# Optimization experiments

Hardware: AMD Instinct MI355X
Metric: run time of the kernel (lower is better)

Reference implementation:

```python
import jax, jax.numpy as jnp
import numpy as np

B, C, HK, WK = 1, 128, 32, 32
S = 4                       # upsample factor hq/hk = dilation
HQ, WQ = HK * S, WK * S
NH = 4                      # heads
HD = C // NH                # head dim
KH = KW = 7                 # odd(max(3, round(2*0.1*32)))
DH = DW = S
EPS = float(jnp.finfo(jnp.float32).eps)  # torch RMSNorm default eps for fp32


def natten_indices(L, K, D):
    """NATTEN clamped-window key indices per query position. Returns [L, K] int array."""
    NS = K // 2
    i = np.arange(L)
    if D <= 1:
        start = np.maximum(i - NS, 0) + (i + NS >= L) * (L - i - NS - 1)
    else:
        ni = i - NS * D
        imodd = i % D
        a = (L // D) * D
        b = L - a
        far = np.where(imodd < b, L - b + imodd - 2 * NS * D, a + imodd - K * D)
        start = np.where(ni < 0, imodd, np.where(i + NS * D >= L, far, ni))
    return jnp.asarray(start[:, None] + np.arange(K)[None, :] * D)


def setup_inputs() -> dict:
    key = jax.random.key(0)
    ks = jax.random.split(key, 8)
    sc = 1.0 / np.sqrt(C)
    return {
        "q": jax.random.normal(ks[0], (B, C, HQ, WQ), jnp.float32),
        "k": jax.random.normal(ks[1], (B, C, HK, WK), jnp.float32),
        "v": jax.random.normal(ks[2], (B, C, HK, WK), jnp.float32),
        "conv_w": jax.random.normal(ks[3], (C, C, 3, 3), jnp.float32) * (sc / 3.0),
        "normq_w": 1.0 + 0.02 * jax.random.normal(ks[4], (C,), jnp.float32),
        "normk_w": 1.0 + 0.02 * jax.random.normal(ks[5], (C,), jnp.float32),
        "qproj_w": jax.random.normal(ks[6], (C, C), jnp.float32) * sc,
        "qproj_b": jnp.zeros((C,), jnp.float32),
        "kproj_w": jax.random.normal(ks[7], (C, C), jnp.float32) * sc,
        "kproj_b": jnp.zeros((C,), jnp.float32),
    }


def _rmsnorm(x, w):  # x: [B,C,H,W]; RMS over channel dim
    ms = jnp.mean(x * x, axis=1, keepdims=True)
    return x * jax.lax.rsqrt(ms + EPS) * w[None, :, None, None]


def reference(q, k, v, conv_w, normq_w, normk_w, qproj_w, qproj_b, kproj_w, kproj_b):
    # 3x3 conv on q (no bias, padding=1)
    q = jax.lax.conv_general_dilated(q, conv_w, (1, 1), "SAME",
                                     dimension_numbers=("NCHW", "OIHW", "NCHW"))
    q = _rmsnorm(q, normq_w)
    k = _rmsnorm(k, normk_w)
    # 1x1 projections (Conv2d k=1 with bias)
    q = jnp.einsum("oc,bchw->bohw", qproj_w, q) + qproj_b[None, :, None, None]
    k = jnp.einsum("oc,bchw->bohw", kproj_w, k) + kproj_b[None, :, None, None]
    # nearest-exact upsample of k, v to (HQ, WQ); integer factor -> exact pixel repeat
    k = jnp.repeat(jnp.repeat(k, S, axis=2), S, axis=3)
    v = jnp.repeat(jnp.repeat(v, S, axis=2), S, axis=3)
    # NATTEN layout [B, H, W, heads, hd]
    qn = q.reshape(B, NH, HD, HQ, WQ).transpose(0, 3, 4, 1, 2)
    kn = k.reshape(B, NH, HD, HQ, WQ).transpose(0, 3, 4, 1, 2)
    vh = v.transpose(0, 2, 3, 1)  # [B,HQ,WQ,C]; V is shared (expanded) across heads.
    # channel-pad-to-8 in the original is a no-op here since C % 8 == 0.
    ih = natten_indices(HQ, KH, DH)  # [HQ, KH]
    iw = natten_indices(WQ, KW, DW)  # [WQ, KW]
    k_nb = jnp.take(jnp.take(kn, ih, axis=1), iw, axis=3)  # [B,HQ,KH,WQ,KW,NH,HD]
    v_nb = jnp.take(jnp.take(vh, ih, axis=1), iw, axis=3)  # [B,HQ,KH,WQ,KW,C]
    scale = HD ** -0.5
    logits = jnp.einsum("bijhd,bimjnhd->bijhmn", qn, k_nb) * scale
    attn = jax.nn.softmax(logits.reshape(B, HQ, WQ, NH, KH * KW), axis=-1)
    attn = attn.reshape(B, HQ, WQ, NH, KH, KW)
    # heads share V, and the block takes mean over heads at the end; the mean
    # commutes with the (linear) V-contraction, so average attention first.
    attn_mean = attn.mean(axis=3)  # [B,HQ,WQ,KH,KW]
    out = jnp.einsum("bijmn,bimjnc->bcij", attn_mean, v_nb)  # [B,C,HQ,WQ]
    return out
```

## Files before the change

kernel.cpp:

```cpp
#include <hip/hip_runtime.h>

#define EPS_ 1.1920928955078125e-07f
#define SCALE_ 0.17677669529663687f

typedef __attribute__((ext_vector_type(8))) short s8b;
typedef __attribute__((ext_vector_type(4))) float f32x4;

static __device__ __forceinline__ unsigned short f2bf(float f) {
  unsigned int u = __float_as_uint(f);
  unsigned int r = (u + 0x7fffu + ((u >> 16) & 1u)) >> 16;
  return (unsigned short)r;
}
static __device__ __forceinline__ float b2fs(short h) {
  return __uint_as_float(((unsigned int)(unsigned short)h) << 16);
}
static __device__ __forceinline__ int S_(int c) {
  return (c < 3) ? 0 : ((c > 28) ? 25 : (c - 3));
}

__global__ __launch_bounds__(256) void prep_k(
    const float* __restrict__ q_in, const float* __restrict__ k_in,
    const float* __restrict__ conv_w, const float* __restrict__ normq_w,
    const float* __restrict__ normk_w, const float* __restrict__ qproj_w,
    const float* __restrict__ kproj_w, const float* __restrict__ kbias,
    unsigned short* __restrict__ qb, unsigned short* __restrict__ kpb,
    unsigned short* __restrict__ wb, unsigned short* __restrict__ wnq) {
  __shared__ __align__(16) char smem[53504];
  unsigned short* t_l = (unsigned short*)smem;
  unsigned short* x_l = (unsigned short*)smem;
  unsigned short* wnk_l = (unsigned short*)(smem + 17408);
  float* red_l = (float*)(smem + 52224);
  float* rs_l  = (float*)(smem + 53248);
  const int b = blockIdx.x, tid = threadIdx.x;
  const int w = tid >> 6, lane = tid & 63;
  const int lm = lane & 15, kg = lane >> 4;

  if (b < 256) {
    const int px0 = b * 64;
    for (int i = tid; i < 2048; i += 256) {
      int c = i >> 4, f = i & 15;
      float4 v = *(const float4*)&q_in[c * 16384 + px0 + f * 4];
      t_l[(f * 4 + 0) * 136 + c] = f2bf(v.x);
      t_l[(f * 4 + 1) * 136 + c] = f2bf(v.y);
      t_l[(f * 4 + 2) * 136 + c] = f2bf(v.z);
      t_l[(f * 4 + 3) * 136 + c] = f2bf(v.w);
    }
    __syncthreads();
    for (int i = tid; i < 1024; i += 256) {
      int p = i >> 4, s = i & 15;
      int px = px0 + p;
      int opx = px + 2 * (px >> 7) + 131;
      *(s8b*)&qb[opx * 128 + s * 8] = *(const s8b*)&t_l[p * 136 + s * 8];
    }
  } else if (b < 265) {
    int gid = (b - 256) * 256 + tid;
    s8b z = {0, 0, 0, 0, 0, 0, 0, 0};
    for (int j = gid; j < 2080; j += 2304) {
      *(s8b*)&qb[j * 8] = z;
      *(s8b*)&qb[129 * 130 * 128 + j * 8] = z;
    }
    for (int j = gid; j < 2048; j += 2304) {
      int r = (j >> 4) + 1, s = j & 15;
      *(s8b*)&qb[(r * 130) * 128 + s * 8] = z;
      *(s8b*)&qb[(r * 130 + 129) * 128 + s * 8] = z;
    }
  } else if (b < 281) {
    const int px0 = (b - 265) * 64;
    for (int i = tid; i < 2048; i += 256) {
      int c = i >> 4, f = i & 15;
      float4 v = *(const float4*)&k_in[c * 1024 + px0 + f * 4];
      x_l[(f * 4 + 0) * 136 + c] = f2bf(v.x);
      x_l[(f * 4 + 1) * 136 + c] = f2bf(v.y);
      x_l[(f * 4 + 2) * 136 + c] = f2bf(v.z);
      x_l[(f * 4 + 3) * 136 + c] = f2bf(v.w);
    }
    for (int i = tid; i < 16384; i += 256) {
      int o = i >> 7, c = i & 127;
      wnk_l[o * 136 + c] = f2bf(kproj_w[i] * normk_w[c]);
    }
    __syncthreads();
    {
      int px = tid >> 2, t4 = tid & 3;
      float ssum = 0.f;
#pragma unroll
      for (int j = 0; j < 4; j++) {
        s8b v = *(const s8b*)&x_l[px * 136 + t4 * 32 + j * 8];
#pragma unroll
        for (int e = 0; e < 8; e++) { float f = b2fs(v[e]); ssum += f * f; }
      }
      red_l[px * 4 + t4] = ssum;
    }
    __syncthreads();
    if (tid < 64)
      rs_l[tid] = rsqrtf((red_l[4 * tid] + red_l[4 * tid + 1] + red_l[4 * tid + 2] +
                          red_l[4 * tid + 3]) * (1.f / 128.f) + EPS_);
    __syncthreads();
    f32x4 acc[2][4];
#pragma unroll
    for (int a = 0; a < 2; a++)
#pragma unroll
      for (int n = 0; n < 4; n++) acc[a][n] = (f32x4){0.f, 0.f, 0.f, 0.f};
#pragma unroll
    for (int kc = 0; kc < 4; kc++) {
      s8b a0 = *(const s8b*)&wnk_l[(2 * w * 16 + lm) * 136 + kc * 32 + kg * 8];
      s8b a1 = *(const s8b*)&wnk_l[((2 * w + 1) * 16 + lm) * 136 + kc * 32 + kg * 8];
#pragma unroll
      for (int nt = 0; nt < 4; nt++) {
        s8b bf = *(const s8b*)&x_l[(nt * 16 + lm) * 136 + kc * 32 + kg * 8];
        acc[0][nt] = __builtin_amdgcn_mfma_f32_16x16x32_bf16(a0, bf, acc[0][nt], 0, 0, 0);
        acc[1][nt] = __builtin_amdgcn_mfma_f32_16x16x32_bf16(a1, bf, acc[1][nt], 0, 0, 0);
      }
    }
    __syncthreads();
#pragma unroll
    for (int mi = 0; mi < 2; mi++)
#pragma unroll
      for (int nt = 0; nt < 4; nt++)
#pragma unroll
        for (int r = 0; r < 4; r++) {
          int px = nt * 16 + lm, c = (2 * w + mi) * 16 + kg * 4 + r;
          x_l[px * 136 + c] = f2bf(kbias[c] + rs_l[px] * acc[mi][nt][r]);
        }
    __syncthreads();
    for (int i = tid; i < 1024; i += 256) {
      int px = i >> 4, s = i & 15;
      *(s8b*)&kpb[(px0 + px) * 128 + s * 8] = *(const s8b*)&x_l[px * 136 + s * 8];
    }
  } else {
    int idx = (b - 281) * 256 + tid;
    if (idx < 147456) {
      int i32 = idx & 31, r = idx >> 5;
      int oc = r & 127, r2 = r >> 7;
      int kc = r2 & 3, t = r2 >> 2;
      wb[idx] = f2bf(conv_w[oc * 1152 + (kc * 32 + i32) * 9 + t]);
    } else {
      int j = idx - 147456;
      wnq[j] = f2bf(qproj_w[j] * normq_w[j & 127]);
    }
  }
}

__global__ __launch_bounds__(512) void fused_k(
    const unsigned short* __restrict__ qb, const unsigned short* __restrict__ kpb,
    const float* __restrict__ v_in, const unsigned short* __restrict__ wb,
    const unsigned short* __restrict__ wnq, const float* __restrict__ qbias,
    float* __restrict__ out) {
  __shared__ __align__(16) char smem[65344];
  unsigned short* in_l = (unsigned short*)smem;
  unsigned short* qc_l = (unsigned short*)smem;
  unsigned short* a_l  = (unsigned short*)smem;
  float* o_l   = (float*)smem;
  unsigned short* kx_l = (unsigned short*)(smem + 27200);
  unsigned short* v_l  = (unsigned short*)(smem + 44608);
  float* red_l = (float*)(smem + 63040);
  float* rs_l  = (float*)(smem + 65088);

  const int tid = threadIdx.x;
  const int CY = blockIdx.x >> 4, CX = blockIdx.x & 15;
  const int Y0 = CY * 8, X0 = CX * 8;
  const int w = tid >> 6, lane = tid & 63;
  const int lm = lane & 15, kg = lane >> 4;
  const int mg = w & 1, ng = w >> 1;
  const int h = w >> 1, mh = w & 1;

  const int sy0 = S_(2 * CY), sy1 = S_(2 * CY + 1);
  const int sx0 = S_(2 * CX), sx1 = S_(2 * CX + 1);
  const int kyb = min(sy0, 24), kxb = min(sx0, 24);
  const int oy0 = sy0 - kyb, oy1 = sy1 - kyb;
  const int ox0 = sx0 - kxb, ox1 = sx1 - kxb;

  for (int i = tid; i < 1600; i += 512) {
    int s = i & 15, r = i >> 4;
    int ry = r / 10, rx = r - ry * 10;
    *(s8b*)&in_l[r * 136 + s * 8] =
        *(const s8b*)&qb[((Y0 + ry) * 130 + X0 + rx) * 128 + s * 8];
  }
  for (int i = tid; i < 1024; i += 512) {
    int j = i >> 4, s = i & 15;
    int ky = j >> 3, kx = j & 7;
    *(s8b*)&kx_l[j * 136 + s * 8] =
        *(const s8b*)&kpb[((kyb + ky) * 32 + kxb + kx) * 128 + s * 8];
  }
  {
    const int j = tid & 63, cg = tid >> 6;
    const int ky = j >> 3, kx = j & 7;
    const float* vp = &v_in[(kyb + ky) * 32 + kxb + kx];
#pragma unroll
    for (int it = 0; it < 16; it++) {
      int c = cg * 16 + it;
      v_l[c * 72 + j] = f2bf(vp[c * 1024]);
    }
  }
  __syncthreads();

  f32x4 acc[4];
#pragma unroll
  for (int a = 0; a < 4; a++) acc[a] = (f32x4){0.f, 0.f, 0.f, 0.f};
  const int pxc = ng * 16 + lm;
  const int qy = pxc >> 3, qx = pxc & 7;
#pragma unroll
  for (int t = 0; t < 9; t++) {
    const int dy = t / 3, dx = t - (t / 3) * 3;
#pragma unroll
    for (int kc = 0; kc < 4; kc++) {
      const unsigned short* wp = wb + (t * 4 + kc) * 4096;
      s8b af[4];
#pragma unroll
      for (int mt = 0; mt < 4; mt++)
        af[mt] = *(const s8b*)&wp[((mg * 4 + mt) * 16 + lm) * 32 + kg * 8];
      s8b bf = *(const s8b*)&in_l[((qy + dy) * 10 + qx + dx) * 136 + kc * 32 + kg * 8];
#pragma unroll
      for (int mt = 0; mt < 4; mt++)
        acc[mt] = __builtin_amdgcn_mfma_f32_16x16x32_bf16(af[mt], bf, acc[mt], 0, 0, 0);
    }
  }
  __syncthreads();
#pragma unroll
  for (int mt = 0; mt < 4; mt++)
#pragma unroll
    for (int r = 0; r < 4; r++) {
      int c = (mg * 4 + mt) * 16 + kg * 4 + r;
      qc_l[pxc * 136 + c] = f2bf(acc[mt][r]);
    }
  __syncthreads();

  {
    int px = tid >> 3, t8 = tid & 7;
    const unsigned short* row = &qc_l[px * 136 + t8 * 16];
    s8b v0 = *(const s8b*)row;
    s8b v1 = *(const s8b*)(row + 8);
    float s = 0.f;
#pragma unroll
    for (int e = 0; e < 8; e++) {
      float f0 = b2fs(v0[e]), f1 = b2fs(v1[e]);
      s += f0 * f0 + f1 * f1;
    }
    red_l[px * 8 + t8] = s;
  }
  __syncthreads();
  if (tid < 64) {
    float s = 0.f;
#pragma unroll
    for (int e = 0; e < 8; e++) s += red_l[tid * 8 + e];
    rs_l[tid] = rsqrtf(s * (1.f / 128.f) + EPS_);
  }
  __syncthreads();

  {
    f32x4 qa[4];
#pragma unroll
    for (int a = 0; a < 4; a++) qa[a] = (f32x4){0.f, 0.f, 0.f, 0.f};
#pragma unroll
    for (int kc = 0; kc < 4; kc++) {
      s8b af[4];
#pragma unroll
      for (int mt = 0; mt < 4; mt++)
        af[mt] = *(const s8b*)&wnq[((mg * 4 + mt) * 16 + lm) * 128 + kc * 32 + kg * 8];
      s8b bf = *(const s8b*)&qc_l[pxc * 136 + kc * 32 + kg * 8];
#pragma unroll
      for (int mt = 0; mt < 4; mt++)
        qa[mt] = __builtin_amdgcn_mfma_f32_16x16x32_bf16(af[mt], bf, qa[mt], 0, 0, 0);
    }
    __syncthreads();
    const float rs = rs_l[pxc];
#pragma unroll
    for (int mt = 0; mt < 4; mt++)
#pragma unroll
      for (int r = 0; r < 4; r++) {
        int c = (mg * 4 + mt) * 16 + kg * 4 + r;
        qc_l[pxc * 136 + c] = f2bf(qbias[c] + rs * qa[mt][r]);
      }
  }
  __syncthreads();

  f32x4 lg[2][4];
  {
    s8b qa[2], kb[4];
#pragma unroll
    for (int mt = 0; mt < 2; mt++)
      qa[mt] = *(const s8b*)&qc_l[((mh * 2 + mt) * 16 + lm) * 136 + h * 32 + kg * 8];
#pragma unroll
    for (int nt = 0; nt < 4; nt++)
      kb[nt] = *(const s8b*)&kx_l[(nt * 16 + lm) * 136 + h * 32 + kg * 8];
#pragma unroll
    for (int mt = 0; mt < 2; mt++)
#pragma unroll
      for (int nt = 0; nt < 4; nt++)
        lg[mt][nt] = __builtin_amdgcn_mfma_f32_16x16x32_bf16(
            qa[mt], kb[nt], (f32x4){0.f, 0.f, 0.f, 0.f}, 0, 0, 0);
  }
  __syncthreads();

  {
    const int kyA = lm >> 3, kxq = lm & 7;
    const bool kxv0 = (unsigned)(kxq - ox0) < 7u;
    const bool kxv1 = (unsigned)(kxq - ox1) < 7u;
#pragma unroll
    for (int mt = 0; mt < 2; mt++) {
#pragma unroll
      for (int r = 0; r < 4; r++) {
        int j = (mh * 2 + mt) * 16 + kg * 4 + r;
        int oy = ((j >> 5) & 1) ? oy1 : oy0;
        bool kxv = ((j >> 2) & 1) ? kxv1 : kxv0;
        float l[4];
#pragma unroll
        for (int nt = 0; nt < 4; nt++) {
          int ky = 2 * nt + kyA;
          bool valid = kxv && ((unsigned)(ky - oy) < 7u);
          l[nt] = valid ? lg[mt][nt][r] * SCALE_ : -1e30f;
        }
        float mx = fmaxf(fmaxf(l[0], l[1]), fmaxf(l[2], l[3]));
#pragma unroll
        for (int off = 1; off < 16; off <<= 1) mx = fmaxf(mx, __shfl_xor(mx, off, 64));
        float e0 = __expf(l[0] - mx), e1 = __expf(l[1] - mx);
        float e2 = __expf(l[2] - mx), e3 = __expf(l[3] - mx);
        float ss = e0 + e1 + e2 + e3;
#pragma unroll
        for (int off = 1; off < 16; off <<= 1) ss += __shfl_xor(ss, off, 64);
        float inv = 1.f / ss;
        unsigned short* ap = &a_l[(h * 64 + j) * 72];
        ap[lm]      = f2bf(e0 * inv);
        ap[16 + lm] = f2bf(e1 * inv);
        ap[32 + lm] = f2bf(e2 * inv);
        ap[48 + lm] = f2bf(e3 * inv);
      }
    }
  }
  __syncthreads();

  f32x4 oacc[4];
#pragma unroll
  for (int a = 0; a < 4; a++) oacc[a] = (f32x4){0.f, 0.f, 0.f, 0.f};
#pragma unroll
  for (int kc = 0; kc < 2; kc++) {
    s8b vb2 = *(const s8b*)&v_l[(w * 16 + lm) * 72 + kc * 32 + kg * 8];
#pragma unroll
    for (int hh = 0; hh < 4; hh++) {
#pragma unroll
      for (int mt = 0; mt < 4; mt++) {
        s8b pa = *(const s8b*)&a_l[(hh * 64 + mt * 16 + lm) * 72 + kc * 32 + kg * 8];
        oacc[mt] = __builtin_amdgcn_mfma_f32_16x16x32_bf16(pa, vb2, oacc[mt], 0, 0, 0);
      }
    }
  }
  __syncthreads();

#pragma unroll
  for (int mt = 0; mt < 4; mt++)
#pragma unroll
    for (int r = 0; r < 4; r++)
      o_l[(w * 16 + lm) * 68 + mt * 16 + kg * 4 + r] = 0.25f * oacc[mt][r];
  __syncthreads();
  for (int i = tid; i < 2048; i += 512) {
    int c = i >> 4, rr = i & 15;
    int qyo = rr >> 1, hx = rr & 1;
    float4 v = *(const float4*)&o_l[c * 68 + qyo * 8 + hx * 4];
    *(float4*)&out[c * 16384 + (Y0 + qyo) * 128 + X0 + hx * 4] = v;
  }
}

extern "C" void kernel_launch(void* const* d_in, const int* in_sizes, int n_in,
                              void* d_out, int out_size, void* d_ws, size_t ws_size,
                              hipStream_t stream) {
  const float* q_in    = (const float*)d_in[0];
  const float* k_in    = (const float*)d_in[1];
  const float* v_in    = (const float*)d_in[2];
  const float* conv_w  = (const float*)d_in[3];
  const float* normq_w = (const float*)d_in[4];
  const float* normk_w = (const float*)d_in[5];
  const float* qproj_w = (const float*)d_in[6];
  const float* qproj_b = (const float*)d_in[7];
  const float* kproj_w = (const float*)d_in[8];
  const float* kproj_b = (const float*)d_in[9];
  float* out = (float*)d_out;

  char* ws = (char*)d_ws;
  unsigned short* qb  = (unsigned short*)(ws);
  unsigned short* kpb = (unsigned short*)(ws + 4326400);
  unsigned short* wb  = (unsigned short*)(ws + 4588544);
  unsigned short* wnq = (unsigned short*)(ws + 4883456);

  prep_k<<<dim3(921), 256, 0, stream>>>(q_in, k_in, conv_w, normq_w, normk_w,
                                        qproj_w, kproj_w, kproj_b,
                                        qb, kpb, wb, wnq);
  fused_k<<<dim3(256), 512, 0, stream>>>(qb, kpb, v_in, wb, wnq, qproj_b, out);
}
```

Measured before the change: 118.9 us.

## Halve fused tile to 8x4 and read bf16 V and K directly from global

```diff
diff --git a/kernel.cpp b/kernel.cpp
--- a/kernel.cpp
+++ b/kernel.cpp
@@ -17,14 +17,22 @@
 static __device__ __forceinline__ int S_(int c) {
   return (c < 3) ? 0 : ((c > 28) ? 25 : (c - 3));
 }
+static __device__ __forceinline__ s8b ld8h(const unsigned short* p) {
+  const unsigned int* u = (const unsigned int*)p;
+  union { unsigned int u4[4]; s8b v; } r;
+  r.u4[0] = u[0]; r.u4[1] = u[1]; r.u4[2] = u[2]; r.u4[3] = u[3];
+  return r.v;
+}
 
 __global__ __launch_bounds__(256) void prep_k(
     const float* __restrict__ q_in, const float* __restrict__ k_in,
-    const float* __restrict__ conv_w, const float* __restrict__ normq_w,
-    const float* __restrict__ normk_w, const float* __restrict__ qproj_w,
-    const float* __restrict__ kproj_w, const float* __restrict__ kbias,
+    const float* __restrict__ v_in, const float* __restrict__ conv_w,
+    const float* __restrict__ normq_w, const float* __restrict__ normk_w,
+    const float* __restrict__ qproj_w, const float* __restrict__ kproj_w,
+    const float* __restrict__ kbias,
     unsigned short* __restrict__ qb, unsigned short* __restrict__ kpb,
-    unsigned short* __restrict__ wb, unsigned short* __restrict__ wnq) {
+    unsigned short* __restrict__ vt, unsigned short* __restrict__ wb,
+    unsigned short* __restrict__ wnq) {
   __shared__ __align__(16) char smem[53504];
   unsigned short* t_l = (unsigned short*)smem;
   unsigned short* x_l = (unsigned short*)smem;
@@ -126,8 +134,18 @@
       int px = i >> 4, s = i & 15;
       *(s8b*)&kpb[(px0 + px) * 128 + s * 8] = *(const s8b*)&x_l[px * 136 + s * 8];
     }
+  } else if (b < 345) {
+    int base = (b - 281) * 2048 + tid * 8;
+    float4 v0 = *(const float4*)&v_in[base];
+    float4 v1 = *(const float4*)&v_in[base + 4];
+    s8b o;
+    o[0] = (short)f2bf(v0.x); o[1] = (short)f2bf(v0.y);
+    o[2] = (short)f2bf(v0.z); o[3] = (short)f2bf(v0.w);
+    o[4] = (short)f2bf(v1.x); o[5] = (short)f2bf(v1.y);
+    o[6] = (short)f2bf(v1.z); o[7] = (short)f2bf(v1.w);
+    *(s8b*)&vt[base] = o;
   } else {
-    int idx = (b - 281) * 256 + tid;
+    int idx = (b - 345) * 256 + tid;
     if (idx < 147456) {
       int i32 = idx & 31, r = idx >> 5;
       int oc = r & 127, r2 = r >> 7;
@@ -140,64 +158,46 @@
   }
 }
 
-__global__ __launch_bounds__(512) void fused_k(
+__global__ __launch_bounds__(256, 4) void fused_k(
     const unsigned short* __restrict__ qb, const unsigned short* __restrict__ kpb,
-    const float* __restrict__ v_in, const unsigned short* __restrict__ wb,
+    const unsigned short* __restrict__ vt, const unsigned short* __restrict__ wb,
     const unsigned short* __restrict__ wnq, const float* __restrict__ qbias,
     float* __restrict__ out) {
-  __shared__ __align__(16) char smem[65344];
+  __shared__ __align__(16) char smem[19584];
   unsigned short* in_l = (unsigned short*)smem;
   unsigned short* qc_l = (unsigned short*)smem;
   unsigned short* a_l  = (unsigned short*)smem;
   float* o_l   = (float*)smem;
-  unsigned short* kx_l = (unsigned short*)(smem + 27200);
-  unsigned short* v_l  = (unsigned short*)(smem + 44608);
-  float* red_l = (float*)(smem + 63040);
-  float* rs_l  = (float*)(smem + 65088);
+  float* red_l = (float*)(smem + 18432);
+  float* rs_l  = (float*)(smem + 19456);
 
   const int tid = threadIdx.x;
-  const int CY = blockIdx.x >> 4, CX = blockIdx.x & 15;
-  const int Y0 = CY * 8, X0 = CX * 8;
+  const int TY = blockIdx.x >> 5, TX = blockIdx.x & 31;
+  const int Y0 = TY * 8, X0 = TX * 4;
   const int w = tid >> 6, lane = tid & 63;
   const int lm = lane & 15, kg = lane >> 4;
   const int mg = w & 1, ng = w >> 1;
-  const int h = w >> 1, mh = w & 1;
-
-  const int sy0 = S_(2 * CY), sy1 = S_(2 * CY + 1);
-  const int sx0 = S_(2 * CX), sx1 = S_(2 * CX + 1);
-  const int kyb = min(sy0, 24), kxb = min(sx0, 24);
+
+  const int sy0 = S_(2 * TY), sy1 = S_(2 * TY + 1);
+  const int sx  = S_(TX);
+  const int kyb = min(sy0, 24);
+  const int kxb = sx & ~1;
   const int oy0 = sy0 - kyb, oy1 = sy1 - kyb;
-  const int ox0 = sx0 - kxb, ox1 = sx1 - kxb;
-
-  for (int i = tid; i < 1600; i += 512) {
+  const int ox  = sx - kxb;
+
+  for (int i = tid; i < 960; i += 256) {
     int s = i & 15, r = i >> 4;
-    int ry = r / 10, rx = r - ry * 10;
+    int ry = r / 6, rx = r - ry * 6;
     *(s8b*)&in_l[r * 136 + s * 8] =
         *(const s8b*)&qb[((Y0 + ry) * 130 + X0 + rx) * 128 + s * 8];
   }
-  for (int i = tid; i < 1024; i += 512) {
-    int j = i >> 4, s = i & 15;
-    int ky = j >> 3, kx = j & 7;
-    *(s8b*)&kx_l[j * 136 + s * 8] =
-        *(const s8b*)&kpb[((kyb + ky) * 32 + kxb + kx) * 128 + s * 8];
-  }
-  {
-    const int j = tid & 63, cg = tid >> 6;
-    const int ky = j >> 3, kx = j & 7;
-    const float* vp = &v_in[(kyb + ky) * 32 + kxb + kx];
-#pragma unroll
-    for (int it = 0; it < 16; it++) {
-      int c = cg * 16 + it;
-      v_l[c * 72 + j] = f2bf(vp[c * 1024]);
-    }
-  }
   __syncthreads();
 
   f32x4 acc[4];
 #pragma unroll
   for (int a = 0; a < 4; a++) acc[a] = (f32x4){0.f, 0.f, 0.f, 0.f};
   const int pxc = ng * 16 + lm;
-  const int qy = pxc >> 3, qx = pxc & 7;
+  const int qy = pxc >> 2, qx = pxc & 3;
 #pragma unroll
   for (int t = 0; t < 9; t++) {
     const int dy = t / 3, dx = t - (t / 3) * 3;
@@ -208,7 +208,7 @@
 #pragma unroll
       for (int mt = 0; mt < 4; mt++)
         af[mt] = *(const s8b*)&wp[((mg * 4 + mt) * 16 + lm) * 32 + kg * 8];
-      s8b bf = *(const s8b*)&in_l[((qy + dy) * 10 + qx + dx) * 136 + kc * 32 + kg * 8];
+      s8b bf = *(const s8b*)&in_l[((qy + dy) * 6 + qx + dx) * 136 + kc * 32 + kg * 8];
 #pragma unroll
       for (int mt = 0; mt < 4; mt++)
         acc[mt] = __builtin_amdgcn_mfma_f32_16x16x32_bf16(af[mt], bf, acc[mt], 0, 0, 0);
@@ -238,7 +238,7 @@
     red_l[px * 8 + t8] = s;
   }
   __syncthreads();
-  if (tid < 64) {
+  if (tid < 32) {
     float s = 0.f;
 #pragma unroll
     for (int e = 0; e < 8; e++) s += red_l[tid * 8 + e];
@@ -273,15 +273,19 @@
   }
   __syncthreads();
 
+  const int h = w;
   f32x4 lg[2][4];
   {
     s8b qa[2], kb[4];
 #pragma unroll
     for (int mt = 0; mt < 2; mt++)
-      qa[mt] = *(const s8b*)&qc_l[((mh * 2 + mt) * 16 + lm) * 136 + h * 32 + kg * 8];
-#pragma unroll
-    for (int nt = 0; nt < 4; nt++)
-      kb[nt] = *(const s8b*)&kx_l[(nt * 16 + lm) * 136 + h * 32 + kg * 8];
+      qa[mt] = *(const s8b*)&qc_l[(mt * 16 + lm) * 136 + h * 32 + kg * 8];
+#pragma unroll
+    for (int nt = 0; nt < 4; nt++) {
+      int n = nt * 16 + lm;
+      int kyL = n >> 3, kxL = n & 7;
+      kb[nt] = *(const s8b*)&kpb[((kyb + kyL) * 32 + kxb + kxL) * 128 + h * 32 + kg * 8];
+    }
 #pragma unroll
     for (int mt = 0; mt < 2; mt++)
 #pragma unroll
@@ -293,15 +297,13 @@
 
   {
     const int kyA = lm >> 3, kxq = lm & 7;
-    const bool kxv0 = (unsigned)(kxq - ox0) < 7u;
-    const bool kxv1 = (unsigned)(kxq - ox1) < 7u;
+    const bool kxv = (unsigned)(kxq - ox) < 7u;
 #pragma unroll
     for (int mt = 0; mt < 2; mt++) {
 #pragma unroll
       for (int r = 0; r < 4; r++) {
-        int j = (mh * 2 + mt) * 16 + kg * 4 + r;
-        int oy = ((j >> 5) & 1) ? oy1 : oy0;
-        bool kxv = ((j >> 2) & 1) ? kxv1 : kxv0;
+        int j = mt * 16 + kg * 4 + r;
+        int oy = ((j >> 4) & 1) ? oy1 : oy0;
         float l[4];
 #pragma unroll
         for (int nt = 0; nt < 4; nt++) {
@@ -318,7 +320,7 @@
 #pragma unroll
         for (int off = 1; off < 16; off <<= 1) ss += __shfl_xor(ss, off, 64);
         float inv = 1.f / ss;
-        unsigned short* ap = &a_l[(h * 64 + j) * 72];
+        unsigned short* ap = &a_l[(h * 32 + j) * 72];
         ap[lm]      = f2bf(e0 * inv);
         ap[16 + lm] = f2bf(e1 * inv);
         ap[32 + lm] = f2bf(e2 * inv);
@@ -328,34 +330,44 @@
   }
   __syncthreads();
 
-  f32x4 oacc[4];
-#pragma unroll
-  for (int a = 0; a < 4; a++) oacc[a] = (f32x4){0.f, 0.f, 0.f, 0.f};
+  f32x4 oacc[2][2];
+#pragma unroll
+  for (int a = 0; a < 2; a++)
+#pragma unroll
+    for (int n = 0; n < 2; n++) oacc[a][n] = (f32x4){0.f, 0.f, 0.f, 0.f};
 #pragma unroll
   for (int kc = 0; kc < 2; kc++) {
-    s8b vb2 = *(const s8b*)&v_l[(w * 16 + lm) * 72 + kc * 32 + kg * 8];
+    s8b vb2[2];
+#pragma unroll
+    for (int nt2 = 0; nt2 < 2; nt2++) {
+      int c = w * 32 + nt2 * 16 + lm;
+      vb2[nt2] = ld8h(&vt[c * 1024 + (kyb + kc * 4 + kg) * 32 + kxb]);
+    }
 #pragma unroll
     for (int hh = 0; hh < 4; hh++) {
 #pragma unroll
-      for (int mt = 0; mt < 4; mt++) {
-        s8b pa = *(const s8b*)&a_l[(hh * 64 + mt * 16 + lm) * 72 + kc * 32 + kg * 8];
-        oacc[mt] = __builtin_amdgcn_mfma_f32_16x16x32_bf16(pa, vb2, oacc[mt], 0, 0, 0);
+      for (int mt = 0; mt < 2; mt++) {
+        s8b pa = *(const s8b*)&a_l[(hh * 32 + mt * 16 + lm) * 72 + kc * 32 + kg * 8];
+#pragma unroll
+        for (int nt2 = 0; nt2 < 2; nt2++)
+          oacc[mt][nt2] = __builtin_amdgcn_mfma_f32_16x16x32_bf16(pa, vb2[nt2], oacc[mt][nt2], 0, 0, 0);
       }
     }
   }
   __syncthreads();
 
 #pragma unroll
-  for (int mt = 0; mt < 4; mt++)
-#pragma unroll
-    for (int r = 0; r < 4; r++)
-      o_l[(w * 16 + lm) * 68 + mt * 16 + kg * 4 + r] = 0.25f * oacc[mt][r];
-  __syncthreads();
-  for (int i = tid; i < 2048; i += 512) {
-    int c = i >> 4, rr = i & 15;
-    int qyo = rr >> 1, hx = rr & 1;
-    float4 v = *(const float4*)&o_l[c * 68 + qyo * 8 + hx * 4];
-    *(float4*)&out[c * 16384 + (Y0 + qyo) * 128 + X0 + hx * 4] = v;
+  for (int mt = 0; mt < 2; mt++)
+#pragma unroll
+    for (int nt2 = 0; nt2 < 2; nt2++)
+#pragma unroll
+      for (int r = 0; r < 4; r++)
+        o_l[(w * 32 + nt2 * 16 + lm) * 36 + mt * 16 + kg * 4 + r] = 0.25f * oacc[mt][nt2][r];
+  __syncthreads();
+  for (int i = tid; i < 1024; i += 256) {
+    int c = i >> 3, qyo = i & 7;
+    float4 v = *(const float4*)&o_l[c * 36 + qyo * 4];
+    *(float4*)&out[c * 16384 + (Y0 + qyo) * 128 + X0] = v;
   }
 }
 
@@ -377,11 +389,12 @@
   char* ws = (char*)d_ws;
   unsigned short* qb  = (unsigned short*)(ws);
   unsigned short* kpb = (unsigned short*)(ws + 4326400);
-  unsigned short* wb  = (unsigned short*)(ws + 4588544);
-  unsigned short* wnq = (unsigned short*)(ws + 4883456);
-
-  prep_k<<<dim3(921), 256, 0, stream>>>(q_in, k_in, conv_w, normq_w, normk_w,
+  unsigned short* vt  = (unsigned short*)(ws + 4588544);
+  unsigned short* wb  = (unsigned short*)(ws + 4850688);
+  unsigned short* wnq = (unsigned short*)(ws + 5145600);
+
+  prep_k<<<dim3(985), 256, 0, stream>>>(q_in, k_in, v_in, conv_w, normq_w, normk_w,
                                         qproj_w, kproj_w, kproj_b,
-                                        qb, kpb, wb, wnq);
-  fused_k<<<dim3(256), 512, 0, stream>>>(qb, kpb, v_in, wb, wnq, qproj_b, out);
-}
+                                        qb, kpb, vt, wb, wnq);
+  fused_k<<<dim3(512), 256, 0, stream>>>(qb, kpb, vt, wb, wnq, qproj_b, out);
+}
```

Result: slower. 121.6 us (+2.3%).
